# Kernel tuning notes

Hardware: AMD Instinct MI355X
Metric: run time of the kernel (lower is better)

Reference implementation:

```python
import jax, jax.numpy as jnp
import numpy as np


def _lstm_step(x, h, c, Wih, Whh, bih, bhh):
    # PyTorch LSTMCell gate order: i, f, g, o
    g = x @ Wih.T + bih + h @ Whh.T + bhh
    i, f, gg, o = jnp.split(g, 4, axis=1)
    c = jax.nn.sigmoid(f) * c + jax.nn.sigmoid(i) * jnp.tanh(gg)
    h = jax.nn.sigmoid(o) * jnp.tanh(c)
    return h, c


def _canvas2seq(canvas):
    # Valid objects (row-sum >= 0) compacted to the front, rest padded with -1.
    mask = canvas.sum(axis=2) >= 0                       # [B, 25]
    order = jnp.argsort(jnp.where(mask, 0, 1), axis=1, stable=True)
    gathered = jnp.take_along_axis(canvas, order[:, :, None], axis=1)
    smask = jnp.take_along_axis(mask, order, axis=1)
    return jnp.where(smask[:, :, None], gathered, jnp.float32(-1.0))


def _canvas_encode(canvas, Wobj, bobj, ce_Wih, ce_Whh, ce_bih, ce_bhh):
    seq = _canvas2seq(canvas)                            # [B, 25, 4]
    x = seq @ Wobj.T + bobj                              # [B, 25, 64]
    B = x.shape[0]
    h = jnp.zeros((B, 64), x.dtype)
    c = jnp.zeros((B, 64), x.dtype)

    def step(carry, xt):
        h, c = carry
        h, c = _lstm_step(xt, h, c, ce_Wih, ce_Whh, ce_bih, ce_bhh)
        return (h, c), None

    (h, _), _ = jax.lax.scan(step, (h, c), jnp.swapaxes(x, 0, 1))
    return h


def setup_inputs() -> dict:
    key = jax.random.key(0)
    ks = jax.random.split(key, 16)
    B, T, V = 256, 65, 10000
    IN, H = 64, 128
    s = 0.05
    inp = {}
    inp["inst"] = jax.random.randint(ks[0], (B, T), 0, V)
    inp["prev_canvas"] = jax.random.uniform(ks[1], (B, 25, 4), dtype=jnp.float32)
    inp["final_canvas"] = jax.random.uniform(ks[2], (B, 25, 4), dtype=jnp.float32)
    inp["target_obj"] = jax.random.normal(ks[3], (B, 4), dtype=jnp.float32)
    inp["embed_W"] = jax.random.normal(ks[4], (V + 1, IN), dtype=jnp.float32) * s
    inp["Wih"] = jax.random.normal(ks[5], (4 * H, IN), dtype=jnp.float32) * s
    inp["Whh"] = jax.random.normal(ks[6], (4 * H, H), dtype=jnp.float32) * s
    inp["bih"] = jnp.zeros((4 * H,), jnp.float32)
    inp["bhh"] = jnp.zeros((4 * H,), jnp.float32)
    inp["Wout"] = jax.random.normal(ks[7], (V + 1, H), dtype=jnp.float32) * s
    inp["bout"] = jnp.zeros((V + 1,), jnp.float32)
    inp["Wtgt"] = jax.random.normal(ks[8], (IN, 4), dtype=jnp.float32) * s
    inp["btgt"] = jnp.zeros((IN,), jnp.float32)
    inp["Wobj"] = jax.random.normal(ks[9], (64, 4), dtype=jnp.float32) * s
    inp["bobj"] = jnp.zeros((64,), jnp.float32)
    inp["ce_Wih"] = jax.random.normal(ks[10], (256, 64), dtype=jnp.float32) * s
    inp["ce_Whh"] = jax.random.normal(ks[11], (256, 64), dtype=jnp.float32) * s
    inp["ce_bih"] = jnp.zeros((256,), jnp.float32)
    inp["ce_bhh"] = jnp.zeros((256,), jnp.float32)
    return inp


def reference(inst, prev_canvas, final_canvas, target_obj,
              embed_W, Wih, Whh, bih, bhh, Wout, bout,
              Wtgt, btgt, Wobj, bobj, ce_Wih, ce_Whh, ce_bih, ce_bhh):
    B, H = inst.shape[0], 128
    tgt_emb = target_obj @ Wtgt.T + btgt                 # [B, 64]
    enc = (_canvas_encode(prev_canvas, Wobj, bobj, ce_Wih, ce_Whh, ce_bih, ce_bhh)
           + _canvas_encode(final_canvas, Wobj, bobj, ce_Wih, ce_Whh, ce_bih, ce_bhh))
    h = jnp.zeros((B, H), jnp.float32)
    c = jnp.zeros((B, H), jnp.float32)
    h, c = _lstm_step(enc, h, c, Wih, Whh, bih, bhh)
    h, c = _lstm_step(tgt_emb, h, c, Wih, Whh, bih, bhh)

    tokens = inst[:, :-1].T                              # [T-1, B]

    def step(carry, it):
        h, c = carry
        xt = embed_W[it]                                 # [B, 64]
        h, c = _lstm_step(xt, h, c, Wih, Whh, bih, bhh)
        lp = jax.nn.log_softmax(h @ Wout.T + bout, axis=1)
        return (h, c), lp

    _, lps = jax.lax.scan(step, (h, c), tokens)          # [T-1, B, V+1]
    return jnp.swapaxes(lps, 0, 1)                       # [B, T-1, V+1]
```

## Files before the change

kernel.cpp:

```cpp
#include <hip/hip_runtime.h>
#include <stdint.h>

typedef __attribute__((ext_vector_type(4))) float f32x4;
typedef __attribute__((ext_vector_type(8))) short s16x8;
typedef __attribute__((ext_vector_type(8))) unsigned short us8;

__device__ __forceinline__ float bf2f(unsigned short u){
  union { unsigned int i; float f; } v; v.i = ((unsigned int)u) << 16; return v.f;
}
__device__ __forceinline__ unsigned short f2bf(float f){
  union { float f; unsigned int i; } v; v.f = f;
  unsigned int r = v.i + 0x7FFFu + ((v.i >> 16) & 1u);
  return (unsigned short)(r >> 16);
}
__device__ __forceinline__ float sigm(float x){ return 1.0f / (1.0f + __expf(-x)); }

#define NA (10240*128)
#define NB 10240
#define ND 512
#define NE (256*64)
#define NF 32768

__global__ void k_prep(const float* __restrict__ Wout, const float* __restrict__ bout,
                       const float* __restrict__ bih,  const float* __restrict__ bhh,
                       const float* __restrict__ tobj, const float* __restrict__ Wtgt,
                       const float* __restrict__ btgt,
                       const float* __restrict__ ceWih, const float* __restrict__ ceWhh,
                       unsigned short* __restrict__ WoutP, float* __restrict__ boutP,
                       float* __restrict__ bsum, float* __restrict__ tgt,
                       unsigned short* __restrict__ cePack)
{
  int tid = blockIdx.x * 256 + threadIdx.x;
  if (tid < NA){
    int vv = tid >> 7, k = tid & 127;
    float val = (vv < 10001) ? Wout[vv*128 + k] : 0.0f;
    WoutP[tid] = f2bf(val);
  } else if (tid < NA+NB){
    int vv = tid - NA;
    boutP[vv] = (vv < 10001) ? bout[vv] : -1e30f;
  } else if (tid < NA+NB+ND){
    int g = tid - NA - NB;
    bsum[g] = bih[g] + bhh[g];
  } else if (tid < NA+NB+ND+NE){
    int i = tid - NA - NB - ND; int b = i >> 6, j = i & 63;
    const float* to = tobj + b*4; const float* wt = Wtgt + j*4;
    tgt[i] = btgt[j] + to[0]*wt[0] + to[1]*wt[1] + to[2]*wt[2] + to[3]*wt[3];
  } else if (tid < NA+NB+ND+NE+NF){
    int i = tid - NA - NB - ND - NE;
    int half = i >> 14;
    int r = (i >> 6) & 255;
    int k = i & 63;
    int k8 = k >> 3;
    int slot = ((k8 ^ (r & 7)) << 3) | (k & 7);
    const float* src = half ? ceWhh : ceWih;
    cePack[half*16384 + r*64 + slot] = f2bf(src[r*64 + k]);
  }
}

__global__ __launch_bounds__(256) void k_canvas(
    const float* __restrict__ prevC, const float* __restrict__ finC,
    const float* __restrict__ Wobj,  const float* __restrict__ bobj,
    const unsigned short* __restrict__ cePack,
    const float* __restrict__ cebih, const float* __restrict__ cebhh,
    float* __restrict__ encP, float* __restrict__ encF)
{
  __shared__ unsigned short wih[256*64] __attribute__((aligned(16)));
  __shared__ unsigned short whh[256*64] __attribute__((aligned(16)));
  __shared__ float seq[25*4];
  __shared__ float xb[64] __attribute__((aligned(16)));
  __shared__ float hb[2][64] __attribute__((aligned(16)));
  __shared__ float gates[256];
  __shared__ float wobj_s[256];
  __shared__ float bobj_s[64];
  __shared__ float bsum_ce[256];

  int tid = threadIdx.x;
  int b = blockIdx.x & 255;
  int which = blockIdx.x >> 8;
  const float* canvas = (which ? finC : prevC) + b*100;

  {
    const us8* cp = (const us8*)cePack;
    us8* wl = (us8*)wih;
    us8* hl = (us8*)whh;
    for (int i = tid; i < 2048; i += 256){
      wl[i] = cp[i];
      hl[i] = cp[2048 + i];
    }
  }
  wobj_s[tid] = Wobj[tid];
  if (tid < 64) bobj_s[tid] = bobj[tid];
  bsum_ce[tid] = cebih[tid] + cebhh[tid];
  if (tid < 64) hb[0][tid] = 0.0f;
  if (tid == 0){
    int pos = 0;
    for (int i = 0; i < 25; i++){
      float a0=canvas[i*4+0], a1=canvas[i*4+1], a2=canvas[i*4+2], a3=canvas[i*4+3];
      if (a0+a1+a2+a3 >= 0.0f){
        seq[pos*4+0]=a0; seq[pos*4+1]=a1; seq[pos*4+2]=a2; seq[pos*4+3]=a3; pos++;
      }
    }
    for (; pos < 25; pos++){
      seq[pos*4+0]=-1.0f; seq[pos*4+1]=-1.0f; seq[pos*4+2]=-1.0f; seq[pos*4+3]=-1.0f;
    }
  }
  __syncthreads();

  float creg = 0.0f;
  int cur = 0;
  const float4* x4 = (const float4*)xb;

  for (int t = 0; t < 25; t++){
    if (tid < 64){
      float a = bobj_s[tid];
      a += wobj_s[tid*4+0]*seq[t*4+0] + wobj_s[tid*4+1]*seq[t*4+1]
         + wobj_s[tid*4+2]*seq[t*4+2] + wobj_s[tid*4+3]*seq[t*4+3];
      xb[tid] = a;
    }
    __syncthreads();
    float acc = bsum_ce[tid];
    const float4* h4 = (const float4*)hb[cur];
    int rowoff = tid*64;
    int sw = tid & 7;
    #pragma unroll
    for (int k8 = 0; k8 < 8; k8++){
      int slot = ((k8 ^ sw) * 8);
      us8 w1 = *reinterpret_cast<const us8*>(&wih[rowoff + slot]);
      us8 w2 = *reinterpret_cast<const us8*>(&whh[rowoff + slot]);
      float4 xa = x4[2*k8], xc = x4[2*k8+1];
      float4 ha = h4[2*k8], hc = h4[2*k8+1];
      acc += bf2f(w1[0])*xa.x + bf2f(w1[1])*xa.y + bf2f(w1[2])*xa.z + bf2f(w1[3])*xa.w;
      acc += bf2f(w1[4])*xc.x + bf2f(w1[5])*xc.y + bf2f(w1[6])*xc.z + bf2f(w1[7])*xc.w;
      acc += bf2f(w2[0])*ha.x + bf2f(w2[1])*ha.y + bf2f(w2[2])*ha.z + bf2f(w2[3])*ha.w;
      acc += bf2f(w2[4])*hc.x + bf2f(w2[5])*hc.y + bf2f(w2[6])*hc.z + bf2f(w2[7])*hc.w;
    }
    gates[tid] = acc;
    __syncthreads();
    if (tid < 64){
      float i_ = sigm(gates[tid]);
      float f_ = sigm(gates[64+tid]);
      float g_ = tanhf(gates[128+tid]);
      float o_ = sigm(gates[192+tid]);
      creg = f_*creg + i_*g_;
      hb[cur^1][tid] = o_ * tanhf(creg);
    }
    __syncthreads();
    cur ^= 1;
  }
  if (tid < 64){
    (which ? encF : encP)[b*64 + tid] = hb[cur][tid];
  }
}

__global__ __launch_bounds__(512, 2) void k_rec(
    const float* __restrict__ Whh, const float* __restrict__ Wih,
    const float* __restrict__ bsum, const int* __restrict__ inst,
    const float* __restrict__ embW, const float* __restrict__ tgt,
    const float* __restrict__ encP, const float* __restrict__ encF,
    unsigned short* __restrict__ Hout)
{
  int b = blockIdx.x;
  int g = threadIdx.x;
  __shared__ float xb[2][64] __attribute__((aligned(16)));
  __shared__ float hb[2][128] __attribute__((aligned(16)));
  __shared__ float gates[512];

  float wreg[128];
  float ureg[64];
  {
    const float4* wrow = (const float4*)(Whh + g*128);
    #pragma unroll
    for (int k4 = 0; k4 < 32; k4++){
      float4 w = wrow[k4];
      wreg[4*k4+0]=w.x; wreg[4*k4+1]=w.y; wreg[4*k4+2]=w.z; wreg[4*k4+3]=w.w;
    }
    const float4* urow = (const float4*)(Wih + g*64);
    #pragma unroll
    for (int k4 = 0; k4 < 16; k4++){
      float4 w = urow[k4];
      ureg[4*k4+0]=w.x; ureg[4*k4+1]=w.y; ureg[4*k4+2]=w.z; ureg[4*k4+3]=w.w;
    }
  }
  float bz = bsum[g];
  float creg = 0.0f;
  if (g < 128) hb[0][g] = 0.0f;
  if (g < 64)  xb[0][g] = encP[b*64+g] + encF[b*64+g];
  int cur = 0;
  __syncthreads();

  for (int s = 0; s < 66; s++){
    float a0 = bz, a1 = 0.0f, a2 = 0.0f, a3 = 0.0f;
    const float4* h4 = (const float4*)hb[cur];
    const float4* x4 = (const float4*)xb[cur];
    #pragma unroll
    for (int k4 = 0; k4 < 32; k4 += 4){
      float4 h0 = h4[k4], h1 = h4[k4+1], h2 = h4[k4+2], h3 = h4[k4+3];
      a0 += wreg[4*k4+0]*h0.x + wreg[4*k4+1]*h0.y + wreg[4*k4+2]*h0.z + wreg[4*k4+3]*h0.w;
      a1 += wreg[4*k4+4]*h1.x + wreg[4*k4+5]*h1.y + wreg[4*k4+6]*h1.z + wreg[4*k4+7]*h1.w;
      a2 += wreg[4*k4+8]*h2.x + wreg[4*k4+9]*h2.y + wreg[4*k4+10]*h2.z + wreg[4*k4+11]*h2.w;
      a3 += wreg[4*k4+12]*h3.x + wreg[4*k4+13]*h3.y + wreg[4*k4+14]*h3.z + wreg[4*k4+15]*h3.w;
    }
    #pragma unroll
    for (int k4 = 0; k4 < 16; k4 += 4){
      float4 x0 = x4[k4], x1 = x4[k4+1], x2 = x4[k4+2], x3 = x4[k4+3];
      a0 += ureg[4*k4+0]*x0.x + ureg[4*k4+1]*x0.y + ureg[4*k4+2]*x0.z + ureg[4*k4+3]*x0.w;
      a1 += ureg[4*k4+4]*x1.x + ureg[4*k4+5]*x1.y + ureg[4*k4+6]*x1.z + ureg[4*k4+7]*x1.w;
      a2 += ureg[4*k4+8]*x2.x + ureg[4*k4+9]*x2.y + ureg[4*k4+10]*x2.z + ureg[4*k4+11]*x2.w;
      a3 += ureg[4*k4+12]*x3.x + ureg[4*k4+13]*x3.y + ureg[4*k4+14]*x3.z + ureg[4*k4+15]*x3.w;
    }
    gates[g] = (a0 + a1) + (a2 + a3);
    __syncthreads();
    if (g < 128){
      float i_ = sigm(gates[g]);
      float f_ = sigm(gates[128+g]);
      float g_ = tanhf(gates[256+g]);
      float o_ = sigm(gates[384+g]);
      creg = f_*creg + i_*g_;
      float h = o_ * tanhf(creg);
      hb[cur^1][g] = h;
      if (s >= 2) Hout[((size_t)(b*64 + (s-2)))*128 + g] = f2bf(h);
    } else if (g < 192 && s < 65){
      int l = g - 128;
      float v;
      if (s + 1 == 1) v = tgt[b*64 + l];
      else { int tok = inst[b*65 + (s - 1)]; v = embW[tok*64 + l]; }
      xb[cur^1][l] = v;
    }
    __syncthreads();
    cur ^= 1;
  }
}

__global__ __launch_bounds__(512, 4) void k_out(
    const unsigned short* __restrict__ Hout, const unsigned short* __restrict__ WoutP,
    const float* __restrict__ boutP, float* __restrict__ out)
{
  extern __shared__ float stage[];
  __shared__ float rs_l[8][32];
  __shared__ float lse_l[32];

  int blk = blockIdx.x;
  int r0 = blk * 32;
  int tid = threadIdx.x;
  int w = tid >> 6;
  int l = tid & 63;
  int lm = l & 15;
  int lq = l >> 4;
  int kof = lq * 8;
  size_t obase = (size_t)r0 * 10001u;

  s16x8 af0[4], af1[4];
  {
    const s16x8* ap0 = (const s16x8*)(Hout + (size_t)(r0 + lm)*128 + kof);
    const s16x8* ap1 = (const s16x8*)(Hout + (size_t)(r0 + 16 + lm)*128 + kof);
    #pragma unroll
    for (int kk = 0; kk < 4; kk++){ af0[kk] = ap0[kk*4]; af1[kk] = ap1[kk*4]; }
  }

  s16x8 bA[4], bB[4];
#define LOADB(dst, tl) { \
    const s16x8* bp_ = (const s16x8*)(WoutP + (size_t)((tl)*16 + lm)*128 + kof); \
    dst[0] = bp_[0]; dst[1] = bp_[4]; dst[2] = bp_[8]; dst[3] = bp_[12]; }

  float rs0[4] = {0,0,0,0}, rs1[4] = {0,0,0,0};
#define P1COMP(buf, tl) { \
    f32x4 a0_ = {0,0,0,0}, a1_ = {0,0,0,0}; \
    _Pragma("unroll") \
    for (int kk = 0; kk < 4; kk++){ \
      a0_ = __builtin_amdgcn_mfma_f32_16x16x32_bf16(af0[kk], buf[kk], a0_, 0, 0, 0); \
      a1_ = __builtin_amdgcn_mfma_f32_16x16x32_bf16(af1[kk], buf[kk], a1_, 0, 0, 0); } \
    float bo_ = boutP[(tl)*16 + lm]; \
    _Pragma("unroll") \
    for (int i = 0; i < 4; i++){ rs0[i] += __expf(a0_[i] + bo_); rs1[i] += __expf(a1_[i] + bo_); } }

  {
    int tl = w;
    LOADB(bA, tl);
    for (int it = 0; it < 39; it++){
      LOADB(bB, tl + 8);
      P1COMP(bA, tl);
      LOADB(bA, tl + 16);
      P1COMP(bB, tl + 8);
      tl += 16;
    }
    LOADB(bB, tl + 8);
    P1COMP(bA, tl);
    P1COMP(bB, tl + 8);
  }

  #pragma unroll
  for (int i = 0; i < 4; i++){
    float s0 = rs0[i], s1 = rs1[i];
    s0 += __shfl_xor(s0, 1); s0 += __shfl_xor(s0, 2); s0 += __shfl_xor(s0, 4); s0 += __shfl_xor(s0, 8);
    s1 += __shfl_xor(s1, 1); s1 += __shfl_xor(s1, 2); s1 += __shfl_xor(s1, 4); s1 += __shfl_xor(s1, 8);
    rs0[i] = s0; rs1[i] = s1;
  }
  if (lm == 0){
    #pragma unroll
    for (int i = 0; i < 4; i++){
      rs_l[w][lq*4 + i] = rs0[i];
      rs_l[w][16 + lq*4 + i] = rs1[i];
    }
  }
  __syncthreads();
  if (tid < 32){
    float s = rs_l[0][tid] + rs_l[1][tid] + rs_l[2][tid] + rs_l[3][tid]
            + rs_l[4][tid] + rs_l[5][tid] + rs_l[6][tid] + rs_l[7][tid];
    lse_l[tid] = logf(s);
  }
  __syncthreads();
  float ml0[4], ml1[4];
  #pragma unroll
  for (int i = 0; i < 4; i++){ ml0[i] = lse_l[lq*4 + i]; ml1[i] = lse_l[16 + lq*4 + i]; }

#define P2COMP(buf, tl, q) { \
    f32x4 p0_ = {0,0,0,0}, p1_ = {0,0,0,0}; \
    _Pragma("unroll") \
    for (int kk = 0; kk < 4; kk++){ \
      p0_ = __builtin_amdgcn_mfma_f32_16x16x32_bf16(af0[kk], buf[kk], p0_, 0, 0, 0); \
      p1_ = __builtin_amdgcn_mfma_f32_16x16x32_bf16(af1[kk], buf[kk], p1_, 0, 0, 0); } \
    float bo_ = boutP[(tl)*16 + lm]; \
    int colq_ = ((q)*16) + lm; \
    _Pragma("unroll") \
    for (int i = 0; i < 4; i++){ \
      stage[(lq*4 + i)*516 + colq_]      = p0_[i] + bo_ - ml0[i]; \
      stage[(16 + lq*4 + i)*516 + colq_] = p1_[i] + bo_ - ml1[i]; } }

#define BAR() { asm volatile("s_waitcnt lgkmcnt(0)" ::: "memory"); __builtin_amdgcn_s_barrier(); }

  LOADB(bA, w*4);
  for (int c = 0; c < 20; c++){
    int tb = c*32 + w*4;
    LOADB(bB, tb + 1);
    P2COMP(bA, tb + 0, w*4 + 0);
    LOADB(bA, tb + 2);
    P2COMP(bB, tb + 1, w*4 + 1);
    LOADB(bB, tb + 3);
    P2COMP(bA, tb + 2, w*4 + 2);
    if (c < 19) LOADB(bA, (c+1)*32 + w*4);
    P2COMP(bB, tb + 3, w*4 + 3);
    BAR();
    int vbase = c * 512;
    if (c < 19){
      #pragma unroll
      for (int j = 0; j < 32; j++){
        int e = j*512 + tid;
        int row = e >> 9, cc = e & 511;
        __builtin_nontemporal_store(stage[row*516 + cc],
            &out[obase + (size_t)row*10001u + (unsigned)(vbase + cc)]);
      }
    } else {
      #pragma unroll
      for (int j = 0; j < 32; j++){
        int e = j*512 + tid;
        int row = e >> 9, cc = e & 511;
        if (vbase + cc < 10001)
          __builtin_nontemporal_store(stage[row*516 + cc],
              &out[obase + (size_t)row*10001u + (unsigned)(vbase + cc)]);
      }
    }
    BAR();
  }
}

extern "C" void kernel_launch(void* const* d_in, const int* in_sizes, int n_in,
                              void* d_out, int out_size, void* d_ws, size_t ws_size,
                              hipStream_t stream)
{
  (void)in_sizes; (void)n_in; (void)out_size; (void)ws_size;
  const int*   inst    = (const int*)  d_in[0];
  const float* prevC   = (const float*)d_in[1];
  const float* finC    = (const float*)d_in[2];
  const float* tobj    = (const float*)d_in[3];
  const float* embW    = (const float*)d_in[4];
  const float* Wih     = (const float*)d_in[5];
  const float* Whh     = (const float*)d_in[6];
  const float* bih     = (const float*)d_in[7];
  const float* bhh     = (const float*)d_in[8];
  const float* Wout    = (const float*)d_in[9];
  const float* bout    = (const float*)d_in[10];
  const float* Wtgt    = (const float*)d_in[11];
  const float* btgt    = (const float*)d_in[12];
  const float* Wobj    = (const float*)d_in[13];
  const float* bobj    = (const float*)d_in[14];
  const float* ceWih   = (const float*)d_in[15];
  const float* ceWhh   = (const float*)d_in[16];
  const float* cebih   = (const float*)d_in[17];
  const float* cebhh   = (const float*)d_in[18];

  char* ws = (char*)d_ws;
  unsigned short* WoutP = (unsigned short*)(ws + 0);
  float* boutP = (float*)(ws + 2621440);
  float* bsum  = (float*)(ws + 2662400);
  float* tgt   = (float*)(ws + 2664448);
  float* encP  = (float*)(ws + 2729984);
  float* encF  = (float*)(ws + 2795520);
  unsigned short* Hout = (unsigned short*)(ws + 2861056);
  unsigned short* cePack = (unsigned short*)(ws + 7055360);
  float* out = (float*)d_out;

  hipFuncSetAttribute((const void*)k_out,
                      hipFuncAttributeMaxDynamicSharedMemorySize, 66048);

  k_prep  <<<5354, 256, 0, stream>>>(Wout, bout, bih, bhh, tobj, Wtgt, btgt,
                                     ceWih, ceWhh, WoutP, boutP, bsum, tgt, cePack);
  k_canvas<<<512, 256, 0, stream>>>(prevC, finC, Wobj, bobj, cePack,
                                    cebih, cebhh, encP, encF);
  k_rec   <<<256, 512, 0, stream>>>(Whh, Wih, bsum, inst, embW, tgt, encP, encF, Hout);
  k_out   <<<512, 512, 66048, stream>>>(Hout, WoutP, boutP, out);
}
```

Baseline: 624.5 us.

## Process 64 rows per block in output projection to halve Wout reloads

Each k_out block now computes 64 output rows instead of 32, so every Wout tile loaded from global memory feeds four MFMA row groups instead of two. This halves the total weight traffic and the grid size (256 blocks). Loads now use a three-buffer rotation, the stage buffer is doubled (row pitch 520), and the write-out is rewritten as a coalesced per-row loop. The costs are roughly double the LDS use, more registers, lower occupancy (launch bounds 2), and only 256 blocks to cover the GPU.

```diff
diff --git a/kernel.cpp b/kernel.cpp
--- a/kernel.cpp
+++ b/kernel.cpp
@@ -231,16 +231,16 @@
   }
 }
 
-__global__ __launch_bounds__(512, 4) void k_out(
+__global__ __launch_bounds__(512, 2) void k_out(
     const unsigned short* __restrict__ Hout, const unsigned short* __restrict__ WoutP,
     const float* __restrict__ boutP, float* __restrict__ out)
 {
   extern __shared__ float stage[];
-  __shared__ float rs_l[8][32];
-  __shared__ float lse_l[32];
+  __shared__ float rs_l[8][64];
+  __shared__ float lse_l[64];
 
   int blk = blockIdx.x;
-  int r0 = blk * 32;
+  int r0 = blk * 64;
   int tid = threadIdx.x;
   int w = tid >> 6;
   int l = tid & 63;
@@ -249,118 +249,134 @@
   int kof = lq * 8;
   size_t obase = (size_t)r0 * 10001u;
 
-  s16x8 af0[4], af1[4];
-  {
-    const s16x8* ap0 = (const s16x8*)(Hout + (size_t)(r0 + lm)*128 + kof);
-    const s16x8* ap1 = (const s16x8*)(Hout + (size_t)(r0 + 16 + lm)*128 + kof);
-    #pragma unroll
-    for (int kk = 0; kk < 4; kk++){ af0[kk] = ap0[kk*4]; af1[kk] = ap1[kk*4]; }
-  }
-
-  s16x8 bA[4], bB[4];
+  s16x8 af[4][4];
+  #pragma unroll
+  for (int c = 0; c < 4; c++){
+    const s16x8* ap = (const s16x8*)(Hout + (size_t)(r0 + c*16 + lm)*128 + kof);
+    #pragma unroll
+    for (int kk = 0; kk < 4; kk++) af[c][kk] = ap[kk*4];
+  }
+
+  s16x8 b0[4], b1[4], b2[4];
 #define LOADB(dst, tl) { \
     const s16x8* bp_ = (const s16x8*)(WoutP + (size_t)((tl)*16 + lm)*128 + kof); \
     dst[0] = bp_[0]; dst[1] = bp_[4]; dst[2] = bp_[8]; dst[3] = bp_[12]; }
 
-  float rs0[4] = {0,0,0,0}, rs1[4] = {0,0,0,0};
-#define P1COMP(buf, tl) { \
-    f32x4 a0_ = {0,0,0,0}, a1_ = {0,0,0,0}; \
+  float rs[4][4] = {};
+#define P1C(buf, tl) { \
+    f32x4 a0_ = {0,0,0,0}, a1_ = {0,0,0,0}, a2_ = {0,0,0,0}, a3_ = {0,0,0,0}; \
     _Pragma("unroll") \
     for (int kk = 0; kk < 4; kk++){ \
-      a0_ = __builtin_amdgcn_mfma_f32_16x16x32_bf16(af0[kk], buf[kk], a0_, 0, 0, 0); \
-      a1_ = __builtin_amdgcn_mfma_f32_16x16x32_bf16(af1[kk], buf[kk], a1_, 0, 0, 0); } \
+      a0_ = __builtin_amdgcn_mfma_f32_16x16x32_bf16(af[0][kk], buf[kk], a0_, 0, 0, 0); \
+      a1_ = __builtin_amdgcn_mfma_f32_16x16x32_bf16(af[1][kk], buf[kk], a1_, 0, 0, 0); \
+      a2_ = __builtin_amdgcn_mfma_f32_16x16x32_bf16(af[2][kk], buf[kk], a2_, 0, 0, 0); \
+      a3_ = __builtin_amdgcn_mfma_f32_16x16x32_bf16(af[3][kk], buf[kk], a3_, 0, 0, 0); } \
     float bo_ = boutP[(tl)*16 + lm]; \
     _Pragma("unroll") \
-    for (int i = 0; i < 4; i++){ rs0[i] += __expf(a0_[i] + bo_); rs1[i] += __expf(a1_[i] + bo_); } }
+    for (int i = 0; i < 4; i++){ \
+      rs[0][i] += __expf(a0_[i] + bo_); rs[1][i] += __expf(a1_[i] + bo_); \
+      rs[2][i] += __expf(a2_[i] + bo_); rs[3][i] += __expf(a3_[i] + bo_); } }
 
   {
     int tl = w;
-    LOADB(bA, tl);
-    for (int it = 0; it < 39; it++){
-      LOADB(bB, tl + 8);
-      P1COMP(bA, tl);
-      LOADB(bA, tl + 16);
-      P1COMP(bB, tl + 8);
-      tl += 16;
-    }
-    LOADB(bB, tl + 8);
-    P1COMP(bA, tl);
-    P1COMP(bB, tl + 8);
+    LOADB(b0, tl); LOADB(b1, tl + 8);
+    for (int p = 0; p < 26; p++){
+      LOADB(b2, tl + 16); P1C(b0, tl);
+      LOADB(b0, tl + 24); P1C(b1, tl + 8);
+      LOADB(b1, tl + 32); P1C(b2, tl + 16);
+      tl += 24;
+    }
+    P1C(b0, tl);
+    P1C(b1, tl + 8);
   }
 
   #pragma unroll
-  for (int i = 0; i < 4; i++){
-    float s0 = rs0[i], s1 = rs1[i];
-    s0 += __shfl_xor(s0, 1); s0 += __shfl_xor(s0, 2); s0 += __shfl_xor(s0, 4); s0 += __shfl_xor(s0, 8);
-    s1 += __shfl_xor(s1, 1); s1 += __shfl_xor(s1, 2); s1 += __shfl_xor(s1, 4); s1 += __shfl_xor(s1, 8);
-    rs0[i] = s0; rs1[i] = s1;
+  for (int c = 0; c < 4; c++){
+    #pragma unroll
+    for (int i = 0; i < 4; i++){
+      float s = rs[c][i];
+      s += __shfl_xor(s, 1); s += __shfl_xor(s, 2);
+      s += __shfl_xor(s, 4); s += __shfl_xor(s, 8);
+      rs[c][i] = s;
+    }
   }
   if (lm == 0){
     #pragma unroll
-    for (int i = 0; i < 4; i++){
-      rs_l[w][lq*4 + i] = rs0[i];
-      rs_l[w][16 + lq*4 + i] = rs1[i];
-    }
-  }
-  __syncthreads();
-  if (tid < 32){
+    for (int c = 0; c < 4; c++)
+      #pragma unroll
+      for (int i = 0; i < 4; i++)
+        rs_l[w][c*16 + lq*4 + i] = rs[c][i];
+  }
+
+#define T2(c,q) ((c)*32 + w*4 + (q))
+  LOADB(b0, T2(0,0)); LOADB(b1, T2(0,1));
+
+#define BAR() { asm volatile("s_waitcnt lgkmcnt(0)" ::: "memory"); __builtin_amdgcn_s_barrier(); }
+
+  BAR();
+  if (tid < 64){
     float s = rs_l[0][tid] + rs_l[1][tid] + rs_l[2][tid] + rs_l[3][tid]
             + rs_l[4][tid] + rs_l[5][tid] + rs_l[6][tid] + rs_l[7][tid];
     lse_l[tid] = logf(s);
   }
-  __syncthreads();
-  float ml0[4], ml1[4];
+  BAR();
+  float ml[4][4];
   #pragma unroll
-  for (int i = 0; i < 4; i++){ ml0[i] = lse_l[lq*4 + i]; ml1[i] = lse_l[16 + lq*4 + i]; }
-
-#define P2COMP(buf, tl, q) { \
-    f32x4 p0_ = {0,0,0,0}, p1_ = {0,0,0,0}; \
+  for (int c = 0; c < 4; c++)
+    #pragma unroll
+    for (int i = 0; i < 4; i++)
+      ml[c][i] = lse_l[c*16 + lq*4 + i];
+
+#define P2C(buf, tl, q) { \
+    f32x4 a0_ = {0,0,0,0}, a1_ = {0,0,0,0}, a2_ = {0,0,0,0}, a3_ = {0,0,0,0}; \
     _Pragma("unroll") \
     for (int kk = 0; kk < 4; kk++){ \
-      p0_ = __builtin_amdgcn_mfma_f32_16x16x32_bf16(af0[kk], buf[kk], p0_, 0, 0, 0); \
-      p1_ = __builtin_amdgcn_mfma_f32_16x16x32_bf16(af1[kk], buf[kk], p1_, 0, 0, 0); } \
+      a0_ = __builtin_amdgcn_mfma_f32_16x16x32_bf16(af[0][kk], buf[kk], a0_, 0, 0, 0); \
+      a1_ = __builtin_amdgcn_mfma_f32_16x16x32_bf16(af[1][kk], buf[kk], a1_, 0, 0, 0); \
+      a2_ = __builtin_amdgcn_mfma_f32_16x16x32_bf16(af[2][kk], buf[kk], a2_, 0, 0, 0); \
+      a3_ = __builtin_amdgcn_mfma_f32_16x16x32_bf16(af[3][kk], buf[kk], a3_, 0, 0, 0); } \
     float bo_ = boutP[(tl)*16 + lm]; \
-    int colq_ = ((q)*16) + lm; \
+    int colq_ = (w*4 + (q))*16 + lm; \
     _Pragma("unroll") \
     for (int i = 0; i < 4; i++){ \
-      stage[(lq*4 + i)*516 + colq_]      = p0_[i] + bo_ - ml0[i]; \
-      stage[(16 + lq*4 + i)*516 + colq_] = p1_[i] + bo_ - ml1[i]; } }
-
-#define BAR() { asm volatile("s_waitcnt lgkmcnt(0)" ::: "memory"); __builtin_amdgcn_s_barrier(); }
-
-  LOADB(bA, w*4);
-  for (int c = 0; c < 20; c++){
-    int tb = c*32 + w*4;
-    LOADB(bB, tb + 1);
-    P2COMP(bA, tb + 0, w*4 + 0);
-    LOADB(bA, tb + 2);
-    P2COMP(bB, tb + 1, w*4 + 1);
-    LOADB(bB, tb + 3);
-    P2COMP(bA, tb + 2, w*4 + 2);
-    if (c < 19) LOADB(bA, (c+1)*32 + w*4);
-    P2COMP(bB, tb + 3, w*4 + 3);
-    BAR();
-    int vbase = c * 512;
-    if (c < 19){
-      #pragma unroll
-      for (int j = 0; j < 32; j++){
-        int e = j*512 + tid;
-        int row = e >> 9, cc = e & 511;
-        __builtin_nontemporal_store(stage[row*516 + cc],
-            &out[obase + (size_t)row*10001u + (unsigned)(vbase + cc)]);
-      }
-    } else {
-      #pragma unroll
-      for (int j = 0; j < 32; j++){
-        int e = j*512 + tid;
-        int row = e >> 9, cc = e & 511;
-        if (vbase + cc < 10001)
-          __builtin_nontemporal_store(stage[row*516 + cc],
-              &out[obase + (size_t)row*10001u + (unsigned)(vbase + cc)]);
-      }
-    }
-    BAR();
-  }
+      stage[(0*16 + lq*4 + i)*520 + colq_] = a0_[i] + bo_ - ml[0][i]; \
+      stage[(1*16 + lq*4 + i)*520 + colq_] = a1_[i] + bo_ - ml[1][i]; \
+      stage[(2*16 + lq*4 + i)*520 + colq_] = a2_[i] + bo_ - ml[2][i]; \
+      stage[(3*16 + lq*4 + i)*520 + colq_] = a3_[i] + bo_ - ml[3][i]; } }
+
+#define WPHASE(c) { \
+    int vbase_ = (c)*512; \
+    if ((c) < 19){ \
+      _Pragma("unroll 4") \
+      for (int j = 0; j < 64; j++){ \
+        __builtin_nontemporal_store(stage[j*520 + tid], \
+            &out[obase + (size_t)j*10001u + (unsigned)(vbase_ + tid)]); } \
+    } else { \
+      if (tid < 273){ \
+        _Pragma("unroll 4") \
+        for (int j = 0; j < 64; j++){ \
+          __builtin_nontemporal_store(stage[j*520 + tid], \
+              &out[obase + (size_t)j*10001u + (unsigned)(vbase_ + tid)]); } } } }
+
+#define CHUNK(ba,bb,bc,c) { \
+    LOADB(bc, T2(c,2));   P2C(ba, T2(c,0), 0); \
+    LOADB(ba, T2(c,3));   P2C(bb, T2(c,1), 1); \
+    LOADB(bb, T2((c)+1,0)); P2C(bc, T2(c,2), 2); \
+    LOADB(bc, T2((c)+1,1)); P2C(ba, T2(c,3), 3); \
+    BAR(); WPHASE(c); BAR(); }
+
+  for (int cb = 0; cb < 18; cb += 3){
+    CHUNK(b0, b1, b2, cb);
+    CHUNK(b1, b2, b0, cb + 1);
+    CHUNK(b2, b0, b1, cb + 2);
+  }
+  CHUNK(b0, b1, b2, 18);
+  LOADB(b0, T2(19,2)); P2C(b1, T2(19,0), 0);
+  LOADB(b1, T2(19,3)); P2C(b2, T2(19,1), 1);
+  P2C(b0, T2(19,2), 2);
+  P2C(b1, T2(19,3), 3);
+  BAR();
+  WPHASE(19);
 }
 
 extern "C" void kernel_launch(void* const* d_in, const int* in_sizes, int n_in,
@@ -400,12 +416,12 @@
   float* out = (float*)d_out;
 
   hipFuncSetAttribute((const void*)k_out,
-                      hipFuncAttributeMaxDynamicSharedMemorySize, 66048);
+                      hipFuncAttributeMaxDynamicSharedMemorySize, 133120);
 
   k_prep  <<<5354, 256, 0, stream>>>(Wout, bout, bih, bhh, tobj, Wtgt, btgt,
                                      ceWih, ceWhh, WoutP, boutP, bsum, tgt, cePack);
   k_canvas<<<512, 256, 0, stream>>>(prevC, finC, Wobj, bobj, cePack,
                                     cebih, cebhh, encP, encF);
   k_rec   <<<256, 512, 0, stream>>>(Whh, Wih, bsum, inst, embW, tgt, encP, encF, Hout);
-  k_out   <<<512, 512, 66048, stream>>>(Hout, WoutP, boutP, out);
-}
+  k_out   <<<256, 512, 133120, stream>>>(Hout, WoutP, boutP, out);
+}
```

Measured after the change: 529.5 us. 1.18x faster.

## Restructure output kernel: split waves across row halves, smaller stage tile, higher occupancy

Applied to the files above, without the earlier changes.

The output log-softmax kernel now assigns each wave a single 16-row half (two wave groups of four) instead of having every wave process both 16-row halves. The shared staging tile is halved to 256 columns and made static, and launch bounds are raised so more workgroups can be resident. Explicit double-buffered B-fragment prefetching is dropped in favour of simple loads, and nontemporal stores become ordinary stores. Each wave group now loads Wout fragments separately, which doubles B traffic per block, and there are twice as many barrier-separated chunks.

```diff
diff --git a/kernel.cpp b/kernel.cpp
--- a/kernel.cpp
+++ b/kernel.cpp
@@ -231,12 +231,12 @@
   }
 }
 
-__global__ __launch_bounds__(512, 4) void k_out(
+__global__ __launch_bounds__(512, 8) void k_out(
     const unsigned short* __restrict__ Hout, const unsigned short* __restrict__ WoutP,
     const float* __restrict__ boutP, float* __restrict__ out)
 {
-  extern __shared__ float stage[];
-  __shared__ float rs_l[8][32];
+  __shared__ float stage[32*260];
+  __shared__ float rs_l[4][32];
   __shared__ float lse_l[32];
 
   int blk = blockIdx.x;
@@ -247,116 +247,84 @@
   int lm = l & 15;
   int lq = l >> 4;
   int kof = lq * 8;
-  size_t obase = (size_t)r0 * 10001u;
-
-  s16x8 af0[4], af1[4];
+  int wg = w >> 2;
+  int wi = w & 3;
+
+  s16x8 af[4];
   {
-    const s16x8* ap0 = (const s16x8*)(Hout + (size_t)(r0 + lm)*128 + kof);
-    const s16x8* ap1 = (const s16x8*)(Hout + (size_t)(r0 + 16 + lm)*128 + kof);
-    #pragma unroll
-    for (int kk = 0; kk < 4; kk++){ af0[kk] = ap0[kk*4]; af1[kk] = ap1[kk*4]; }
-  }
-
-  s16x8 bA[4], bB[4];
-#define LOADB(dst, tl) { \
-    const s16x8* bp_ = (const s16x8*)(WoutP + (size_t)((tl)*16 + lm)*128 + kof); \
-    dst[0] = bp_[0]; dst[1] = bp_[4]; dst[2] = bp_[8]; dst[3] = bp_[12]; }
-
-  float rs0[4] = {0,0,0,0}, rs1[4] = {0,0,0,0};
-#define P1COMP(buf, tl) { \
-    f32x4 a0_ = {0,0,0,0}, a1_ = {0,0,0,0}; \
-    _Pragma("unroll") \
-    for (int kk = 0; kk < 4; kk++){ \
-      a0_ = __builtin_amdgcn_mfma_f32_16x16x32_bf16(af0[kk], buf[kk], a0_, 0, 0, 0); \
-      a1_ = __builtin_amdgcn_mfma_f32_16x16x32_bf16(af1[kk], buf[kk], a1_, 0, 0, 0); } \
-    float bo_ = boutP[(tl)*16 + lm]; \
-    _Pragma("unroll") \
-    for (int i = 0; i < 4; i++){ rs0[i] += __expf(a0_[i] + bo_); rs1[i] += __expf(a1_[i] + bo_); } }
-
-  {
-    int tl = w;
-    LOADB(bA, tl);
-    for (int it = 0; it < 39; it++){
-      LOADB(bB, tl + 8);
-      P1COMP(bA, tl);
-      LOADB(bA, tl + 16);
-      P1COMP(bB, tl + 8);
-      tl += 16;
-    }
-    LOADB(bB, tl + 8);
-    P1COMP(bA, tl);
-    P1COMP(bB, tl + 8);
+    const s16x8* ap = (const s16x8*)(Hout + (size_t)(r0 + wg*16 + lm)*128 + kof);
+    #pragma unroll
+    for (int kk = 0; kk < 4; kk++) af[kk] = ap[kk*4];
+  }
+
+#define MFMA4(a_, bp_) { \
+    s16x8 q0_ = bp_[0], q1_ = bp_[4], q2_ = bp_[8], q3_ = bp_[12]; \
+    a_ = __builtin_amdgcn_mfma_f32_16x16x32_bf16(af[0], q0_, a_, 0, 0, 0); \
+    a_ = __builtin_amdgcn_mfma_f32_16x16x32_bf16(af[1], q1_, a_, 0, 0, 0); \
+    a_ = __builtin_amdgcn_mfma_f32_16x16x32_bf16(af[2], q2_, a_, 0, 0, 0); \
+    a_ = __builtin_amdgcn_mfma_f32_16x16x32_bf16(af[3], q3_, a_, 0, 0, 0); }
+
+  float rs[4] = {0,0,0,0};
+  for (int t = wi; t < 640; t += 4){
+    const s16x8* bp = (const s16x8*)(WoutP + (size_t)(t*16 + lm)*128 + kof);
+    f32x4 a = {0,0,0,0};
+    MFMA4(a, bp);
+    float bo = boutP[t*16 + lm];
+    #pragma unroll
+    for (int i = 0; i < 4; i++) rs[i] += __expf(a[i] + bo);
   }
 
   #pragma unroll
   for (int i = 0; i < 4; i++){
-    float s0 = rs0[i], s1 = rs1[i];
-    s0 += __shfl_xor(s0, 1); s0 += __shfl_xor(s0, 2); s0 += __shfl_xor(s0, 4); s0 += __shfl_xor(s0, 8);
-    s1 += __shfl_xor(s1, 1); s1 += __shfl_xor(s1, 2); s1 += __shfl_xor(s1, 4); s1 += __shfl_xor(s1, 8);
-    rs0[i] = s0; rs1[i] = s1;
+    float s = rs[i];
+    s += __shfl_xor(s, 1); s += __shfl_xor(s, 2);
+    s += __shfl_xor(s, 4); s += __shfl_xor(s, 8);
+    rs[i] = s;
   }
   if (lm == 0){
     #pragma unroll
-    for (int i = 0; i < 4; i++){
-      rs_l[w][lq*4 + i] = rs0[i];
-      rs_l[w][16 + lq*4 + i] = rs1[i];
-    }
+    for (int i = 0; i < 4; i++) rs_l[wi][wg*16 + lq*4 + i] = rs[i];
   }
   __syncthreads();
-  if (tid < 32){
-    float s = rs_l[0][tid] + rs_l[1][tid] + rs_l[2][tid] + rs_l[3][tid]
-            + rs_l[4][tid] + rs_l[5][tid] + rs_l[6][tid] + rs_l[7][tid];
-    lse_l[tid] = logf(s);
-  }
+  if (tid < 32)
+    lse_l[tid] = logf(rs_l[0][tid] + rs_l[1][tid] + rs_l[2][tid] + rs_l[3][tid]);
   __syncthreads();
-  float ml0[4], ml1[4];
+  float ml[4];
   #pragma unroll
-  for (int i = 0; i < 4; i++){ ml0[i] = lse_l[lq*4 + i]; ml1[i] = lse_l[16 + lq*4 + i]; }
-
-#define P2COMP(buf, tl, q) { \
-    f32x4 p0_ = {0,0,0,0}, p1_ = {0,0,0,0}; \
-    _Pragma("unroll") \
-    for (int kk = 0; kk < 4; kk++){ \
-      p0_ = __builtin_amdgcn_mfma_f32_16x16x32_bf16(af0[kk], buf[kk], p0_, 0, 0, 0); \
-      p1_ = __builtin_amdgcn_mfma_f32_16x16x32_bf16(af1[kk], buf[kk], p1_, 0, 0, 0); } \
-    float bo_ = boutP[(tl)*16 + lm]; \
-    int colq_ = ((q)*16) + lm; \
-    _Pragma("unroll") \
-    for (int i = 0; i < 4; i++){ \
-      stage[(lq*4 + i)*516 + colq_]      = p0_[i] + bo_ - ml0[i]; \
-      stage[(16 + lq*4 + i)*516 + colq_] = p1_[i] + bo_ - ml1[i]; } }
+  for (int i = 0; i < 4; i++) ml[i] = lse_l[wg*16 + lq*4 + i];
 
 #define BAR() { asm volatile("s_waitcnt lgkmcnt(0)" ::: "memory"); __builtin_amdgcn_s_barrier(); }
 
-  LOADB(bA, w*4);
-  for (int c = 0; c < 20; c++){
-    int tb = c*32 + w*4;
-    LOADB(bB, tb + 1);
-    P2COMP(bA, tb + 0, w*4 + 0);
-    LOADB(bA, tb + 2);
-    P2COMP(bB, tb + 1, w*4 + 1);
-    LOADB(bB, tb + 3);
-    P2COMP(bA, tb + 2, w*4 + 2);
-    if (c < 19) LOADB(bA, (c+1)*32 + w*4);
-    P2COMP(bB, tb + 3, w*4 + 3);
+  size_t obase = (size_t)r0 * 10001u;
+  for (int c = 0; c < 40; c++){
+    #pragma unroll
+    for (int q = 0; q < 4; q++){
+      int t = c*16 + wi*4 + q;
+      const s16x8* bp = (const s16x8*)(WoutP + (size_t)(t*16 + lm)*128 + kof);
+      f32x4 a = {0,0,0,0};
+      MFMA4(a, bp);
+      float bo = boutP[t*16 + lm];
+      int colq = (wi*4 + q)*16 + lm;
+      #pragma unroll
+      for (int i = 0; i < 4; i++)
+        stage[(wg*16 + lq*4 + i)*260 + colq] = a[i] + bo - ml[i];
+    }
     BAR();
-    int vbase = c * 512;
-    if (c < 19){
+    int vbase = c * 256;
+    if (c < 39){
       #pragma unroll
-      for (int j = 0; j < 32; j++){
+      for (int j = 0; j < 16; j++){
         int e = j*512 + tid;
-        int row = e >> 9, cc = e & 511;
-        __builtin_nontemporal_store(stage[row*516 + cc],
-            &out[obase + (size_t)row*10001u + (unsigned)(vbase + cc)]);
+        int row = e >> 8, cc = e & 255;
+        out[obase + (size_t)row*10001u + (unsigned)(vbase + cc)] = stage[row*260 + cc];
       }
     } else {
       #pragma unroll
-      for (int j = 0; j < 32; j++){
+      for (int j = 0; j < 16; j++){
         int e = j*512 + tid;
-        int row = e >> 9, cc = e & 511;
-        if (vbase + cc < 10001)
-          __builtin_nontemporal_store(stage[row*516 + cc],
-              &out[obase + (size_t)row*10001u + (unsigned)(vbase + cc)]);
+        int row = e >> 8, cc = e & 255;
+        if (cc < 17)
+          out[obase + (size_t)row*10001u + (unsigned)(vbase + cc)] = stage[row*260 + cc];
       }
     }
     BAR();
@@ -399,13 +367,10 @@
   unsigned short* cePack = (unsigned short*)(ws + 7055360);
   float* out = (float*)d_out;
 
-  hipFuncSetAttribute((const void*)k_out,
-                      hipFuncAttributeMaxDynamicSharedMemorySize, 66048);
-
   k_prep  <<<5354, 256, 0, stream>>>(Wout, bout, bih, bhh, tobj, Wtgt, btgt,
                                      ceWih, ceWhh, WoutP, boutP, bsum, tgt, cePack);
   k_canvas<<<512, 256, 0, stream>>>(prevC, finC, Wobj, bobj, cePack,
                                     cebih, cebhh, encP, encF);
   k_rec   <<<256, 512, 0, stream>>>(Whh, Wih, bsum, inst, embW, tgt, encP, encF, Hout);
-  k_out   <<<512, 512, 66048, stream>>>(Hout, WoutP, boutP, out);
-}
+  k_out   <<<512, 512, 0, stream>>>(Hout, WoutP, boutP, out);
+}
```

Result: slower. 1.038 ms (+66.2%).
